# Kernel tuning notes

Measured on AMD Instinct MI355X. Metric: run time of the kernel, lower is better.

The kernel has to match this reference:

```python
import jax, jax.numpy as jnp
import numpy as np

DIM = 1024
NUM_HEADS = 16
HEAD_DIM = DIM // NUM_HEADS
SCALE = HEAD_DIM ** -0.5
B, N = 2, 2048


def setup_inputs() -> dict:
    key = jax.random.key(0)
    k_x, k_qkv, k_prjw, k_prjb = jax.random.split(key, 4)
    # nn.Linear(dim, 3*dim, bias=False): weight [3*dim, dim]
    s = 1.0 / np.sqrt(DIM)
    return {
        "x": jax.random.normal(k_x, (B, N, DIM), dtype=jnp.float32),
        "w_qkv": jax.random.uniform(k_qkv, (3 * DIM, DIM), jnp.float32, -s, s),
        "w_prj": jax.random.uniform(k_prjw, (DIM, DIM), jnp.float32, -s, s),
        "b_prj": jax.random.uniform(k_prjb, (DIM,), jnp.float32, -s, s),
    }


def reference(x, w_qkv, w_prj, b_prj):
    Bb, Nn, C = x.shape
    qkv = jnp.einsum("bnc,dc->bnd", x, w_qkv)            # [B,N,3C]
    qkv = qkv.reshape(Bb, Nn, 3, NUM_HEADS, HEAD_DIM)
    qkv = jnp.transpose(qkv, (2, 0, 3, 1, 4))            # [3,B,H,N,hd]
    q, k, v = qkv[0], qkv[1], qkv[2]
    attn = jnp.einsum("bhqd,bhkd->bhqk", q, k) * SCALE   # [B,H,N,N]
    attn = jax.nn.softmax(attn, axis=-1)
    out = jnp.einsum("bhqk,bhkd->bhqd", attn, v)         # [B,H,N,hd]
    out = jnp.transpose(out, (0, 2, 1, 3)).reshape(Bb, Nn, C)
    # dropout layers are identity at eval / p=0
    return jnp.einsum("bnc,dc->bnd", out, w_prj) + b_prj
```

## Files before the change

### kernel.cpp

```cpp
#include <hip/hip_runtime.h>

typedef unsigned short u16;
typedef unsigned int u32;
typedef __attribute__((ext_vector_type(8))) short s16x8;
typedef __attribute__((ext_vector_type(4))) short s16x4;
typedef __attribute__((ext_vector_type(4))) float f32x4;

#define DIM    1024
#define NHEADS 16
#define HD     64
#define NSEQ   2048
#define QKVN   3072

__device__ __forceinline__ u16 f2bf(float f) {
  u32 u = __float_as_uint(f);
  u += 0x7FFF + ((u >> 16) & 1);
  return (u16)(u >> 16);
}

__device__ __forceinline__ float vexp2(float x) {
#if __has_builtin(__builtin_amdgcn_exp2f)
  return __builtin_amdgcn_exp2f(x);
#else
  return __expf(x * 0.69314718055994531f);
#endif
}

__device__ __forceinline__ void async16(const u16* g, u16* l) {
  __builtin_amdgcn_global_load_lds(
      (const __attribute__((address_space(1))) unsigned int*)g,
      (__attribute__((address_space(3))) unsigned int*)l, 16, 0, 0);
}

__global__ void cast_all(const float* __restrict__ x, const float* __restrict__ wq,
                         const float* __restrict__ wp, u16* __restrict__ xo,
                         u16* __restrict__ wqo, u16* __restrict__ wpo) {
  int i = blockIdx.x * 256 + threadIdx.x;
  const float4* src; u16* dst; int off;
  if (i < 1048576)      { src = (const float4*)x;  dst = xo;  off = i; }
  else if (i < 1835008) { src = (const float4*)wq; dst = wqo; off = i - 1048576; }
  else                  { src = (const float4*)wp; dst = wpo; off = i - 1835008; }
  float4 f = src[off];
  ushort4 o;
  o.x = f2bf(f.x); o.y = f2bf(f.y); o.z = f2bf(f.z); o.w = f2bf(f.w);
  ((ushort4*)dst)[off] = o;
}

template <bool FINAL>
__global__ __launch_bounds__(256, 3) void gemm_bt(
    const u16* __restrict__ A, const u16* __restrict__ Bw, u16* __restrict__ qkv,
    u16* __restrict__ vt, const float* __restrict__ bias, float* __restrict__ outp) {
  constexpr int K = 1024;
  constexpr int BM = FINAL ? 64 : 128;
  constexpr int MT = FINAL ? 64 : 32;
  constexpr int IT = FINAL ? 2 : 4;
  constexpr int ACALLS = BM / 16;
  constexpr int TCALLS = ACALLS + 8;
  constexpr int PW = TCALLS / 4;
  const int bm = blockIdx.x % MT;
  const int bn = blockIdx.x / MT;
  const int tid = threadIdx.x;
  const int wave = tid >> 6, lane = tid & 63;
  const int q4 = lane >> 4, l15 = lane & 15;
  const int wm = wave >> 1, wn = wave & 1;
  const int m0 = bm * BM, n0 = bn * 128;

  __shared__ alignas(16) u16 lsA[BM * 32];
  __shared__ alignas(16) u16 lsB[128 * 32];

  f32x4 acc[IT][4];
#pragma unroll
  for (int i = 0; i < IT; i++)
#pragma unroll
    for (int j = 0; j < 4; j++) acc[i][j] = (f32x4){0.f, 0.f, 0.f, 0.f};

  for (int k0 = 0; k0 < K; k0 += 32) {
    __syncthreads();
#pragma unroll
    for (int j = 0; j < PW; ++j) {
      int t = wave * PW + j;
      if (t < ACALLS) {
        int lin = t * 64 + lane;
        int r = lin >> 2, c = lin & 3;
        async16(A + (size_t)(m0 + r) * K + k0 + c * 8, lsA + t * 512);
      } else {
        int tb = t - ACALLS;
        int lin = tb * 64 + lane;
        int r = lin >> 2, c = lin & 3;
        async16(Bw + (size_t)(n0 + r) * K + k0 + c * 8, lsB + tb * 512);
      }
    }
    __syncthreads();
    s16x8 af[IT], bfr[4];
#pragma unroll
    for (int i = 0; i < IT; ++i)
      af[i] = *(const s16x8*)(lsA + (wm * (IT * 16) + i * 16 + l15) * 32 + q4 * 8);
#pragma unroll
    for (int j = 0; j < 4; ++j)
      bfr[j] = *(const s16x8*)(lsB + (wn * 64 + j * 16 + l15) * 32 + q4 * 8);
#pragma unroll
    for (int i = 0; i < IT; ++i)
#pragma unroll
      for (int j = 0; j < 4; ++j)
        acc[i][j] = __builtin_amdgcn_mfma_f32_16x16x32_bf16(af[i], bfr[j], acc[i][j], 0, 0, 0);
  }

#pragma unroll
  for (int i = 0; i < IT; i++) {
#pragma unroll
    for (int j = 0; j < 4; j++) {
      int n = n0 + wn * 64 + j * 16 + l15;
      int mb = m0 + wm * (IT * 16) + i * 16 + q4 * 4;
      if (FINAL) {
#pragma unroll
        for (int r = 0; r < 4; r++)
          outp[(size_t)(mb + r) * DIM + n] = acc[i][j][r] + bias[n];
      } else if (n < 2048) {
#pragma unroll
        for (int r = 0; r < 4; r++)
          qkv[(size_t)(mb + r) * QKVN + n] = f2bf(acc[i][j][r]);
      } else {
        int b = mb >> 11, tok = mb & 2047;
        int h = (n >> 6) & 15, hd = n & 63;
        ushort4 pk;
        pk.x = f2bf(acc[i][j][0]); pk.y = f2bf(acc[i][j][1]);
        pk.z = f2bf(acc[i][j][2]); pk.w = f2bf(acc[i][j][3]);
        *(ushort4*)(vt + ((size_t)((b * NHEADS + h) * HD + hd)) * NSEQ + tok) = pk;
      }
    }
  }
}

__global__ __launch_bounds__(256, 2) void attn_kernel(const u16* __restrict__ qkv,
                                                      const u16* __restrict__ vt,
                                                      u16* __restrict__ aout) {
  const int blk = blockIdx.x;
  const int bh = blk & 31, qt = blk >> 5;
  const int b = bh >> 4, h = bh & 15;
  const int tid = threadIdx.x;
  const int wave = tid >> 6, lane = tid & 63;
  const int g = wave >> 1, wq = wave & 1;
  const int q4 = lane >> 4, l15 = lane & 15;

  __shared__ alignas(16) u16 smem[32768];
  u16* lsKb = smem + g * 2 * 4096;
  u16* lsVb = smem + 16384 + g * 2 * 4096;
  float* lsO = (float*)smem;
  float* lsS = lsO + 64 * 132;

  const float QSCALE = 0.18033688011112042f;
  s16x8 aq[4][2];
#pragma unroll
  for (int rt = 0; rt < 4; ++rt)
#pragma unroll
    for (int kc = 0; kc < 2; ++kc) {
      int row = b * NSEQ + qt * 128 + wq * 64 + rt * 16 + l15;
      uint4 d = *(const uint4*)(qkv + (size_t)row * QKVN + h * HD + kc * 32 + q4 * 8);
      u32 w[4] = {d.x, d.y, d.z, d.w};
      s16x8 f;
#pragma unroll
      for (int j = 0; j < 8; ++j) {
        u16 u = (u16)(w[j >> 1] >> ((j & 1) * 16));
        float v = __uint_as_float(((u32)u) << 16) * QSCALE;
        f[j] = (short)f2bf(v);
      }
      aq[rt][kc] = f;
    }

  f32x4 o[4][4];
  float lsum[4] = {0.f, 0.f, 0.f, 0.f};
#pragma unroll
  for (int rt = 0; rt < 4; ++rt)
#pragma unroll
    for (int ht = 0; ht < 4; ++ht) o[rt][ht] = (f32x4){0.f, 0.f, 0.f, 0.f};

  auto stage = [&](int ktl, int buf) {
#pragma unroll
    for (int j = 0; j < 4; ++j) {
      int t = wq * 4 + j;
      int lin = t * 64 + lane;
      int r = lin >> 3, c = (lin & 7) ^ (r & 7);
      int key = g * 1024 + ktl * 64;
      async16(qkv + (size_t)(b * NSEQ + key + r) * QKVN + DIM + h * HD + c * 8,
              lsKb + buf * 4096 + t * 512);
      async16(vt + (size_t)(bh * HD + r) * NSEQ + key + c * 8,
              lsVb + buf * 4096 + t * 512);
    }
  };

  stage(0, 0);

  for (int kt = 0; kt < 16; ++kt) {
    const int buf = kt & 1;
    __syncthreads();
    if (kt + 1 < 16) stage(kt + 1, buf ^ 1);
    const u16* lsK = lsKb + buf * 4096;
    const u16* lsV = lsVb + buf * 4096;

    s16x8 kf[2][4];
#pragma unroll
    for (int kc = 0; kc < 2; ++kc)
#pragma unroll
      for (int ct = 0; ct < 4; ++ct) {
        int r = ct * 16 + l15;
        int c = (kc * 4 + q4) ^ (r & 7);
        kf[kc][ct] = *(const s16x8*)(lsK + r * 64 + c * 8);
      }
    s16x4 vf[4][4];
#pragma unroll
    for (int ct = 0; ct < 4; ++ct)
#pragma unroll
      for (int ht = 0; ht < 4; ++ht) {
        int row = ht * 16 + l15;
        int gch = ct * 2 + (q4 >> 1);
        int p = gch ^ (row & 7);
        vf[ct][ht] = *(const s16x4*)(lsV + row * 64 + p * 8 + (q4 & 1) * 4);
      }

#pragma unroll
    for (int rt = 0; rt < 4; ++rt) {
      f32x4 st[4];
#pragma unroll
      for (int ct = 0; ct < 4; ++ct) st[ct] = (f32x4){0.f, 0.f, 0.f, 0.f};
#pragma unroll
      for (int kc = 0; kc < 2; ++kc)
#pragma unroll
        for (int ct = 0; ct < 4; ++ct)
          st[ct] = __builtin_amdgcn_mfma_f32_16x16x32_bf16(kf[kc][ct], aq[rt][kc], st[ct], 0, 0, 0);

      s16x4 pa[4];
#pragma unroll
      for (int ct = 0; ct < 4; ++ct) {
        u32 u0 = __float_as_uint(vexp2(st[ct][0]));
        u32 u1 = __float_as_uint(vexp2(st[ct][1]));
        u32 u2 = __float_as_uint(vexp2(st[ct][2]));
        u32 u3 = __float_as_uint(vexp2(st[ct][3]));
        lsum[rt] += __uint_as_float(u0 & 0xffff0000u) + __uint_as_float(u1 & 0xffff0000u) +
                    __uint_as_float(u2 & 0xffff0000u) + __uint_as_float(u3 & 0xffff0000u);
        union { u32 w[2]; s16x4 v; } pk;
        pk.w[0] = (u0 >> 16) | (u1 & 0xffff0000u);
        pk.w[1] = (u2 >> 16) | (u3 & 0xffff0000u);
        pa[ct] = pk.v;
      }

#pragma unroll
      for (int ct = 0; ct < 4; ++ct)
#pragma unroll
        for (int ht = 0; ht < 4; ++ht)
          o[rt][ht] = __builtin_amdgcn_mfma_f32_16x16x16bf16_1k(pa[ct], vf[ct][ht], o[rt][ht], 0, 0, 0);
    }
  }

#pragma unroll
  for (int rt = 0; rt < 4; ++rt) {
    lsum[rt] += __shfl_xor(lsum[rt], 16, 64);
    lsum[rt] += __shfl_xor(lsum[rt], 32, 64);
  }

  __syncthreads();
  if (g == 1) {
#pragma unroll
    for (int rt = 0; rt < 4; ++rt) {
#pragma unroll
      for (int ht = 0; ht < 4; ++ht) {
        int addr = (ht * 16 + l15) * 132 + wq * 64 + rt * 16 + q4 * 4;
        *(float4*)(lsO + addr) = (float4){o[rt][ht][0], o[rt][ht][1], o[rt][ht][2], o[rt][ht][3]};
      }
      if (q4 == 0) lsS[wq * 64 + rt * 16 + l15] = lsum[rt];
    }
  }
  __syncthreads();
  if (g == 0) {
#pragma unroll
    for (int rt = 0; rt < 4; ++rt) {
      float4 s2 = *(const float4*)(lsS + wq * 64 + rt * 16 + q4 * 4);
      float inv[4];
      inv[0] = 1.0f / (__shfl(lsum[rt], q4 * 4 + 0, 64) + s2.x);
      inv[1] = 1.0f / (__shfl(lsum[rt], q4 * 4 + 1, 64) + s2.y);
      inv[2] = 1.0f / (__shfl(lsum[rt], q4 * 4 + 2, 64) + s2.z);
      inv[3] = 1.0f / (__shfl(lsum[rt], q4 * 4 + 3, 64) + s2.w);
#pragma unroll
      for (int ht = 0; ht < 4; ++ht) {
        float4 o2 = *(const float4*)(lsO + (ht * 16 + l15) * 132 + wq * 64 + rt * 16 + q4 * 4);
        float v[4] = {o[rt][ht][0] + o2.x, o[rt][ht][1] + o2.y,
                      o[rt][ht][2] + o2.z, o[rt][ht][3] + o2.w};
#pragma unroll
        for (int r = 0; r < 4; ++r) {
          int n = qt * 128 + wq * 64 + rt * 16 + q4 * 4 + r;
          int col = h * HD + ht * 16 + l15;
          aout[(size_t)(b * NSEQ + n) * DIM + col] = f2bf(v[r] * inv[r]);
        }
      }
    }
  }
}

extern "C" void kernel_launch(void* const* d_in, const int* in_sizes, int n_in,
                              void* d_out, int out_size, void* d_ws, size_t ws_size,
                              hipStream_t stream) {
  const float* x     = (const float*)d_in[0];
  const float* w_qkv = (const float*)d_in[1];
  const float* w_prj = (const float*)d_in[2];
  const float* b_prj = (const float*)d_in[3];
  float* out = (float*)d_out;

  char* ws = (char*)d_ws;
  u16* x_bf    = (u16*)(ws);
  u16* wqkv_bf = (u16*)(ws + (size_t)(8u << 20));
  u16* wprj_bf = (u16*)(ws + (size_t)(14u << 20));
  u16* qkv     = (u16*)(ws + (size_t)(16u << 20));
  u16* vt      = (u16*)(ws + (size_t)(40u << 20));
  u16* aout    = (u16*)(ws + (size_t)(48u << 20));

  cast_all<<<8192, 256, 0, stream>>>(x, w_qkv, w_prj, x_bf, wqkv_bf, wprj_bf);
  gemm_bt<false><<<32 * 24, 256, 0, stream>>>(x_bf, wqkv_bf, qkv, vt, nullptr, nullptr);
  attn_kernel<<<512, 256, 0, stream>>>(qkv, vt, aout);
  gemm_bt<true><<<64 * 8, 256, 0, stream>>>(aout, wprj_bf, nullptr, nullptr, b_prj, out);
}
```

Measured before the change: 180.4 us.

## Halve attention LDS staging to raise occupancy and add MFMA wave priority

The attention kernel's shared-memory staging shrinks from two per-group double buffers to one shared double buffer of 32 keys per group per step. The loop now runs 32 iterations with smaller K/V fragments, and launch bounds rise from 2 to 4 blocks per CU. The aim is to fit more blocks per CU so latency is hidden better. s_setprio is placed around the MFMA sections to favour matrix issue. The cost is twice as many barriers and staging rounds, less work per barrier, and tighter register limits that could cause spills.

```diff
diff --git a/kernel.cpp b/kernel.cpp
--- a/kernel.cpp
+++ b/kernel.cpp
@@ -131,7 +131,7 @@
   }
 }
 
-__global__ __launch_bounds__(256, 2) void attn_kernel(const u16* __restrict__ qkv,
+__global__ __launch_bounds__(256, 4) void attn_kernel(const u16* __restrict__ qkv,
                                                       const u16* __restrict__ vt,
                                                       u16* __restrict__ aout) {
   const int blk = blockIdx.x;
@@ -142,9 +142,7 @@
   const int g = wave >> 1, wq = wave & 1;
   const int q4 = lane >> 4, l15 = lane & 15;
 
-  __shared__ alignas(16) u16 smem[32768];
-  u16* lsKb = smem + g * 2 * 4096;
-  u16* lsVb = smem + 16384 + g * 2 * 4096;
+  __shared__ alignas(16) u16 smem[17152];
   float* lsO = (float*)smem;
   float* lsS = lsO + 64 * 132;
 
@@ -175,62 +173,70 @@
     for (int ht = 0; ht < 4; ++ht) o[rt][ht] = (f32x4){0.f, 0.f, 0.f, 0.f};
 
   auto stage = [&](int ktl, int buf) {
+    u16* dstK = smem + buf * 8192;
+    u16* dstV = smem + buf * 8192 + 4096;
 #pragma unroll
     for (int j = 0; j < 4; ++j) {
-      int t = wq * 4 + j;
+      int id = wave * 4 + j;
+      int t = id & 7;
       int lin = t * 64 + lane;
       int r = lin >> 3, c = (lin & 7) ^ (r & 7);
-      int key = g * 1024 + ktl * 64;
-      async16(qkv + (size_t)(b * NSEQ + key + r) * QKVN + DIM + h * HD + c * 8,
-              lsKb + buf * 4096 + t * 512);
-      async16(vt + (size_t)(bh * HD + r) * NSEQ + key + c * 8,
-              lsVb + buf * 4096 + t * 512);
+      if (id < 8) {
+        int key = (r >> 5) * 1024 + ktl * 32 + (r & 31);
+        async16(qkv + (size_t)(b * NSEQ + key) * QKVN + DIM + h * HD + c * 8,
+                dstK + t * 512);
+      } else {
+        int koff = (c >> 2) * 1024 + ktl * 32 + (c & 3) * 8;
+        async16(vt + (size_t)(bh * HD + r) * NSEQ + koff, dstV + t * 512);
+      }
     }
   };
 
   stage(0, 0);
 
-  for (int kt = 0; kt < 16; ++kt) {
+  for (int kt = 0; kt < 32; ++kt) {
     const int buf = kt & 1;
     __syncthreads();
-    if (kt + 1 < 16) stage(kt + 1, buf ^ 1);
-    const u16* lsK = lsKb + buf * 4096;
-    const u16* lsV = lsVb + buf * 4096;
-
-    s16x8 kf[2][4];
+    if (kt + 1 < 32) stage(kt + 1, buf ^ 1);
+    const u16* lsK = smem + buf * 8192;
+    const u16* lsV = smem + buf * 8192 + 4096;
+
+    s16x8 kf[2][2];
 #pragma unroll
     for (int kc = 0; kc < 2; ++kc)
 #pragma unroll
-      for (int ct = 0; ct < 4; ++ct) {
-        int r = ct * 16 + l15;
+      for (int ct = 0; ct < 2; ++ct) {
+        int r = g * 32 + ct * 16 + l15;
         int c = (kc * 4 + q4) ^ (r & 7);
         kf[kc][ct] = *(const s16x8*)(lsK + r * 64 + c * 8);
       }
-    s16x4 vf[4][4];
-#pragma unroll
-    for (int ct = 0; ct < 4; ++ct)
+    s16x4 vf[2][4];
+#pragma unroll
+    for (int ct = 0; ct < 2; ++ct)
 #pragma unroll
       for (int ht = 0; ht < 4; ++ht) {
         int row = ht * 16 + l15;
-        int gch = ct * 2 + (q4 >> 1);
+        int gch = g * 4 + ct * 2 + (q4 >> 1);
         int p = gch ^ (row & 7);
         vf[ct][ht] = *(const s16x4*)(lsV + row * 64 + p * 8 + (q4 & 1) * 4);
       }
 
 #pragma unroll
     for (int rt = 0; rt < 4; ++rt) {
-      f32x4 st[4];
-#pragma unroll
-      for (int ct = 0; ct < 4; ++ct) st[ct] = (f32x4){0.f, 0.f, 0.f, 0.f};
+      f32x4 st[2];
+#pragma unroll
+      for (int ct = 0; ct < 2; ++ct) st[ct] = (f32x4){0.f, 0.f, 0.f, 0.f};
+      __builtin_amdgcn_s_setprio(1);
 #pragma unroll
       for (int kc = 0; kc < 2; ++kc)
 #pragma unroll
-        for (int ct = 0; ct < 4; ++ct)
+        for (int ct = 0; ct < 2; ++ct)
           st[ct] = __builtin_amdgcn_mfma_f32_16x16x32_bf16(kf[kc][ct], aq[rt][kc], st[ct], 0, 0, 0);
-
-      s16x4 pa[4];
-#pragma unroll
-      for (int ct = 0; ct < 4; ++ct) {
+      __builtin_amdgcn_s_setprio(0);
+
+      s16x4 pa[2];
+#pragma unroll
+      for (int ct = 0; ct < 2; ++ct) {
         u32 u0 = __float_as_uint(vexp2(st[ct][0]));
         u32 u1 = __float_as_uint(vexp2(st[ct][1]));
         u32 u2 = __float_as_uint(vexp2(st[ct][2]));
@@ -243,11 +249,13 @@
         pa[ct] = pk.v;
       }
 
-#pragma unroll
-      for (int ct = 0; ct < 4; ++ct)
+      __builtin_amdgcn_s_setprio(1);
+#pragma unroll
+      for (int ct = 0; ct < 2; ++ct)
 #pragma unroll
         for (int ht = 0; ht < 4; ++ht)
           o[rt][ht] = __builtin_amdgcn_mfma_f32_16x16x16bf16_1k(pa[ct], vf[ct][ht], o[rt][ht], 0, 0, 0);
+      __builtin_amdgcn_s_setprio(0);
     }
   }
 
```

Result: slower. 382.3 us (+111.9%).
